# Kernel optimization log

Measured on AMD Instinct MI355X. Metric: run time of the kernel, lower is better.

Reference implementation:

```python
import jax, jax.numpy as jnp
import numpy as np

B, S = 8, 2048
D_IN, D_STATE, D_OUT = 1024, 1024, 1024
H = 16
DH = D_STATE // H  # 64
N_LAYERS = 24
STD = 0.02
EPS = 1e-6


def setup_inputs() -> dict:
    key = jax.random.key(0)
    k = jax.random.split(key, 4)
    x = jax.random.normal(k[0], (B, S, D_IN), dtype=jnp.float32)
    # input_projection: Linear(D_IN, 4*D_STATE, bias=False), std=0.02
    w_in = jax.random.normal(k[1], (D_IN, 4 * D_STATE), dtype=jnp.float32) * STD
    # state_weight: [3*H, DH, DH] recurrence matrices (candidate, forget, reset)
    state_weight = jax.random.normal(k[2], (3 * H, DH, DH), dtype=jnp.float32) * STD
    # rmsnorm weight over state_size
    norm_weight = jnp.ones((D_STATE,), dtype=jnp.float32)
    # output_projection: Linear(D_STATE, D_OUT, bias=False), std scaled by sqrt(2*num_layers)
    w_out = jax.random.normal(k[3], (D_STATE, D_OUT), dtype=jnp.float32) * (STD / np.sqrt(2 * N_LAYERS))
    return {"x": x, "w_in": w_in, "state_weight": state_weight,
            "norm_weight": norm_weight, "w_out": w_out}


def _rmsnorm(x, w):
    var = jnp.mean(jnp.square(x), axis=-1, keepdims=True)
    return x * jax.lax.rsqrt(var + EPS) * w


def reference(x, w_in, state_weight, norm_weight, w_out):
    # input projection -> [B, S, 4*D_STATE]
    proj = jnp.einsum('bsi,io->bso', x, w_in)
    xg, g = jnp.split(proj, [3 * D_STATE], axis=-1)
    xi, xf, xr = jnp.split(xg, 3, axis=-1)
    # per-head views [B, S, H, DH]
    xi = xi.reshape(B, S, H, DH)
    xf = xf.reshape(B, S, H, DH)
    xr = xr.reshape(B, S, H, DH)
    W, Wf, Wr = jnp.split(state_weight, 3, axis=0)  # each [H, DH, DH]

    # scan over time: carry h [B, H, DH]
    def step(h, inp):
        xi_t, xf_t, xr_t = inp  # each [B, H, DH]
        r = jax.nn.sigmoid(xr_t + jnp.einsum('bhd,hde->bhe', h, Wr))
        f = jax.nn.sigmoid(xf_t + jnp.einsum('bhd,hde->bhe', h, Wf))
        c = jnp.tanh(xi_t + jnp.einsum('bhd,hde->bhe', r * h, W))
        h_new = f * h + (1.0 - f) * c
        return h_new, h_new

    h0 = jnp.zeros((B, H, DH), dtype=x.dtype)
    xs = (jnp.swapaxes(xi, 0, 1), jnp.swapaxes(xf, 0, 1), jnp.swapaxes(xr, 0, 1))
    _, hs = jax.lax.scan(step, h0, xs)  # hs: [S, B, H, DH]
    h_seq = jnp.swapaxes(hs, 0, 1).reshape(B, S, D_STATE)

    # gated output: h * silu(g), rmsnorm, output projection
    y = h_seq * jax.nn.silu(g)
    y = _rmsnorm(y, norm_weight)
    return jnp.einsum('bsd,do->bso', y, w_out)
```

## Files before the change

### kernel.cpp

```cpp
#include <hip/hip_runtime.h>
#include <hip/hip_bf16.h>
#include <math.h>

typedef __hip_bfloat16 bf16;

#define B_      8
#define S_      2048
#define DIN     1024
#define DSTATE  1024
#define H_      16
#define DH_     64
#define PROJ4   4096

__device__ __forceinline__ unsigned short f2bf(float f) {
    unsigned int x = __float_as_uint(f);
    x += 0x7FFFu + ((x >> 16) & 1u);
    return (unsigned short)(x >> 16);
}

__device__ __forceinline__ float4 load4(const float* p) { return *(const float4*)p; }
__device__ __forceinline__ float4 load4(const bf16* p) {
    uint2 u = *(const uint2*)p;
    float4 r;
    r.x = __uint_as_float((u.x & 0xFFFFu) << 16);
    r.y = __uint_as_float(u.x & 0xFFFF0000u);
    r.z = __uint_as_float((u.y & 0xFFFFu) << 16);
    r.w = __uint_as_float(u.y & 0xFFFF0000u);
    return r;
}
__device__ __forceinline__ void store4(float* p, float4 v) { *(float4*)p = v; }
__device__ __forceinline__ void store4(bf16* p, float4 v) {
    uint2 u;
    u.x = (unsigned int)f2bf(v.x) | ((unsigned int)f2bf(v.y) << 16);
    u.y = (unsigned int)f2bf(v.z) | ((unsigned int)f2bf(v.w) << 16);
    *(uint2*)p = u;
}

typedef __attribute__((ext_vector_type(8))) short bf16x8;
typedef __attribute__((ext_vector_type(4))) float f32x4;
typedef __attribute__((ext_vector_type(2))) float f32x2;
typedef __attribute__((ext_vector_type(4))) short short4v;

template <typename TA>
__device__ __forceinline__ void load_a4(const TA* p, float out[4]);
template <>
__device__ __forceinline__ void load_a4<float>(const float* p, float out[4]) {
    float4 v = *(const float4*)p;
    out[0] = v.x; out[1] = v.y; out[2] = v.z; out[3] = v.w;
}
template <>
__device__ __forceinline__ void load_a4<bf16>(const bf16* p, float out[4]) {
    float4 v = load4(p);
    out[0] = v.x; out[1] = v.y; out[2] = v.z; out[3] = v.w;
}

template <typename TA, typename TC>
__global__ __launch_bounds__(256) void gemm_mfma(const TA* __restrict__ A,
                                                 const float* __restrict__ Bm,
                                                 TC* __restrict__ C,
                                                 int M, int N, int K, int lda) {
    __shared__ short As[128][40];
    __shared__ short Bs[128][40];

    const int tid = threadIdx.x;
    const int m0 = blockIdx.y * 128;
    const int n0 = blockIdx.x * 128;

    const int saM = tid >> 1;
    const int saK = (tid & 1) * 16;
    const int sbK = tid >> 3;
    const int sbN = (tid & 7) * 16;

    const int wid = tid >> 6;
    const int wx = wid & 1, wy = wid >> 1;
    const int lane = tid & 63;
    const int c16 = lane & 15;
    const int quad = lane >> 4;

    const TA* Aptr = A + (size_t)(m0 + saM) * lda + saK;
    const float* Bptr = Bm + (size_t)sbK * N + n0 + sbN;

    f32x4 acc[4][4];
    #pragma unroll
    for (int i = 0; i < 4; ++i)
        #pragma unroll
        for (int j = 0; j < 4; ++j) acc[i][j] = (f32x4){0.f, 0.f, 0.f, 0.f};

    float ra[4][4];
    float rb[4][4];
    #pragma unroll
    for (int i = 0; i < 4; ++i) load_a4<TA>(Aptr + i * 4, ra[i]);
    #pragma unroll
    for (int i = 0; i < 4; ++i) {
        float4 v = load4(Bptr + i * 4);
        rb[i][0] = v.x; rb[i][1] = v.y; rb[i][2] = v.z; rb[i][3] = v.w;
    }

    for (int k0 = 0; k0 < K; k0 += 32) {
        __syncthreads();
        #pragma unroll
        for (int i = 0; i < 4; ++i) {
            short4v pk = { (short)f2bf(ra[i][0]), (short)f2bf(ra[i][1]),
                           (short)f2bf(ra[i][2]), (short)f2bf(ra[i][3]) };
            *(short4v*)&As[saM][saK + i * 4] = pk;
        }
        #pragma unroll
        for (int i = 0; i < 4; ++i)
            #pragma unroll
            for (int j = 0; j < 4; ++j)
                Bs[sbN + i * 4 + j][sbK] = (short)f2bf(rb[i][j]);
        __syncthreads();

        if (k0 + 32 < K) {
            #pragma unroll
            for (int i = 0; i < 4; ++i) load_a4<TA>(Aptr + k0 + 32 + i * 4, ra[i]);
            #pragma unroll
            for (int i = 0; i < 4; ++i) {
                float4 v = load4(Bptr + (size_t)(k0 + 32) * N + i * 4);
                rb[i][0] = v.x; rb[i][1] = v.y; rb[i][2] = v.z; rb[i][3] = v.w;
            }
        }

        bf16x8 af[4], bfr[4];
        #pragma unroll
        for (int mt = 0; mt < 4; ++mt)
            af[mt] = *(const bf16x8*)&As[wy * 64 + mt * 16 + c16][quad * 8];
        #pragma unroll
        for (int nt = 0; nt < 4; ++nt)
            bfr[nt] = *(const bf16x8*)&Bs[wx * 64 + nt * 16 + c16][quad * 8];

        #pragma unroll
        for (int mt = 0; mt < 4; ++mt)
            #pragma unroll
            for (int nt = 0; nt < 4; ++nt)
                acc[mt][nt] = __builtin_amdgcn_mfma_f32_16x16x32_bf16(
                    af[mt], bfr[nt], acc[mt][nt], 0, 0, 0);
    }

    #pragma unroll
    for (int mt = 0; mt < 4; ++mt) {
        #pragma unroll
        for (int r = 0; r < 4; ++r) {
            int row = m0 + wy * 64 + mt * 16 + quad * 4 + r;
            TC* cp = C + (size_t)row * N + n0 + wx * 64;
            #pragma unroll
            for (int nt = 0; nt < 4; ++nt)
                cp[nt * 16 + c16] = (TC)acc[mt][nt][r];
        }
    }
}

#define RPT32(M) M(0) M(1) M(2) M(3) M(4) M(5) M(6) M(7) M(8) M(9) M(10) M(11) \
  M(12) M(13) M(14) M(15) M(16) M(17) M(18) M(19) M(20) M(21) M(22) M(23) \
  M(24) M(25) M(26) M(27) M(28) M(29) M(30) M(31)

__global__ __launch_bounds__(64, 1) void recur_kernel(bf16* __restrict__ proj,
                                                      const float* __restrict__ sw) {
    const int e = threadIdx.x & 63;
    const int bh = blockIdx.x;
    const int b = bh >> 4;
    const int h = bh & 15;

    __shared__ __align__(16) float lds_h[64];
    __shared__ __align__(16) float lds_rh[64];

    const float* Wc_p = sw + (size_t)h * 4096 + e;
    const float* Wf_p = Wc_p + (size_t)16 * 4096;
    const float* Wr_p = Wc_p + (size_t)32 * 4096;

    #define DECLW(i) f32x2 wr##i, wf##i, wc##i;
    RPT32(DECLW)
    #undef DECLW
    #define LOADW(i) \
        wr##i = (f32x2){Wr_p[(2*i) * 64], Wr_p[(2*i+1) * 64]}; \
        wf##i = (f32x2){Wf_p[(2*i) * 64], Wf_p[(2*i+1) * 64]}; \
        wc##i = (f32x2){Wc_p[(2*i) * 64], Wc_p[(2*i+1) * 64]};
    RPT32(LOADW)
    #undef LOADW

    bf16* xi_p = proj + (size_t)b * S_ * PROJ4 + h * 64 + e;

    f32x4 rxi, rxf, rxr;
    #define PRELOAD(U) { const bf16* p = xi_p + (size_t)(U) * PROJ4; \
        rxi[U] = __bfloat162float(p[0]); \
        rxf[U] = __bfloat162float(p[1024]); \
        rxr[U] = __bfloat162float(p[2048]); }
    PRELOAD(0) PRELOAD(1) PRELOAD(2) PRELOAD(3)
    #undef PRELOAD

    float hreg = 0.0f;
    lds_h[e] = 0.0f;

    const bf16* ld = xi_p + (size_t)4 * PROJ4;
    bf16*       st = xi_p;

    #define P1(J, A, Bq) { \
        f32x4 hb = *(const f32x4*)&lds_h[4 * (J)]; \
        aR0 = __builtin_elementwise_fma(hb.lo, wr##A, aR0); \
        aR1 = __builtin_elementwise_fma(hb.hi, wr##Bq, aR1); \
        aF0 = __builtin_elementwise_fma(hb.lo, wf##A, aF0); \
        aF1 = __builtin_elementwise_fma(hb.hi, wf##Bq, aF1); }
    #define P1_ALL \
        P1(0,0,1)   P1(1,2,3)   P1(2,4,5)   P1(3,6,7) \
        P1(4,8,9)   P1(5,10,11) P1(6,12,13) P1(7,14,15) \
        P1(8,16,17) P1(9,18,19) P1(10,20,21) P1(11,22,23) \
        P1(12,24,25) P1(13,26,27) P1(14,28,29) P1(15,30,31)

    #define P2(J, A, Bq) { \
        f32x4 qb = *(const f32x4*)&lds_rh[4 * (J)]; \
        aC0 = __builtin_elementwise_fma(qb.lo, wc##A, aC0); \
        aC1 = __builtin_elementwise_fma(qb.hi, wc##Bq, aC1); }
    #define P2_ALL \
        P2(0,0,1)   P2(1,2,3)   P2(2,4,5)   P2(3,6,7) \
        P2(4,8,9)   P2(5,10,11) P2(6,12,13) P2(7,14,15) \
        P2(8,16,17) P2(9,18,19) P2(10,20,21) P2(11,22,23) \
        P2(12,24,25) P2(13,26,27) P2(14,28,29) P2(15,30,31)

    #define STEP(U, REFILL) { \
        float xi0 = rxi[U], xf0 = rxf[U], xr0 = rxr[U]; \
        if (REFILL) { \
            const bf16* p = ld + (size_t)(U) * PROJ4; \
            rxi[U] = __bfloat162float(p[0]); \
            rxf[U] = __bfloat162float(p[1024]); \
            rxr[U] = __bfloat162float(p[2048]); \
        } \
        f32x2 aR0 = {0.f, 0.f}, aR1 = {0.f, 0.f}; \
        f32x2 aF0 = {0.f, 0.f}, aF1 = {0.f, 0.f}; \
        P1_ALL \
        f32x2 aR = aR0 + aR1, aF = aF0 + aF1; \
        float sr = xr0 + aR.x + aR.y; \
        float sf = xf0 + aF.x + aF.y; \
        float r = 1.f / (1.f + __expf(-sr)); \
        float f = 1.f / (1.f + __expf(-sf)); \
        float rh = r * hreg; \
        lds_rh[e] = rh; \
        f32x2 aC0 = {0.f, 0.f}, aC1 = {0.f, 0.f}; \
        P2_ALL \
        f32x2 aC = aC0 + aC1; \
        float sc = xi0 + aC.x + aC.y; \
        sc = fminf(fmaxf(sc, -15.f), 15.f); \
        float ex = __expf(-2.f * sc); \
        float cc = (1.f - ex) / (1.f + ex); \
        hreg = f * hreg + (1.f - f) * cc; \
        lds_h[e] = hreg; \
        st[(size_t)(U) * PROJ4] = __float2bfloat16(hreg); \
    }

    for (int t0 = 0; t0 < S_ - 4; t0 += 4) {
        STEP(0, 1) STEP(1, 1) STEP(2, 1) STEP(3, 1)
        ld += (size_t)4 * PROJ4;
        st += (size_t)4 * PROJ4;
    }
    STEP(0, 0) STEP(1, 0) STEP(2, 0) STEP(3, 0)

    #undef STEP
    #undef P1
    #undef P1_ALL
    #undef P2
    #undef P2_ALL
}

__global__ __launch_bounds__(256) void gate_norm_kernel(bf16* __restrict__ proj,
                                                        const float* __restrict__ nw) {
    const int row = blockIdx.x;
    const int tid = threadIdx.x;
    __shared__ float red[4];

    bf16* hp = proj + (size_t)row * PROJ4;
    const bf16* gp = hp + 3 * DSTATE;

    float4 hv = load4(hp + tid * 4);
    float4 gv = load4(gp + tid * 4);

    float v0 = hv.x * (gv.x / (1.f + __expf(-gv.x)));
    float v1 = hv.y * (gv.y / (1.f + __expf(-gv.y)));
    float v2 = hv.z * (gv.z / (1.f + __expf(-gv.z)));
    float v3 = hv.w * (gv.w / (1.f + __expf(-gv.w)));

    float ss = v0 * v0 + v1 * v1 + v2 * v2 + v3 * v3;
    #pragma unroll
    for (int mask = 32; mask >= 1; mask >>= 1)
        ss += __shfl_xor(ss, mask, 64);

    const int wid = tid >> 6;
    if ((tid & 63) == 0) red[wid] = ss;
    __syncthreads();
    float tot = red[0] + red[1] + red[2] + red[3];
    float scale = rsqrtf(tot * (1.0f / (float)DSTATE) + 1e-6f);

    float4 nv = *(const float4*)(nw + tid * 4);
    float4 y;
    y.x = v0 * scale * nv.x;
    y.y = v1 * scale * nv.y;
    y.z = v2 * scale * nv.z;
    y.w = v3 * scale * nv.w;
    store4(hp + tid * 4, y);
}

extern "C" void kernel_launch(void* const* d_in, const int* in_sizes, int n_in,
                              void* d_out, int out_size, void* d_ws, size_t ws_size,
                              hipStream_t stream) {
    const float* x     = (const float*)d_in[0];
    const float* w_in  = (const float*)d_in[1];
    const float* sw    = (const float*)d_in[2];
    const float* nw    = (const float*)d_in[3];
    const float* w_out = (const float*)d_in[4];
    float* out = (float*)d_out;

    bf16* proj = (bf16*)d_ws;

    dim3 g1(PROJ4 / 128, (B_ * S_) / 128);
    gemm_mfma<float, bf16><<<g1, 256, 0, stream>>>(x, w_in, proj,
                                                   B_ * S_, PROJ4, DIN, DIN);

    recur_kernel<<<128, 64, 0, stream>>>(proj, sw);

    gate_norm_kernel<<<B_ * S_, 256, 0, stream>>>(proj, nw);

    dim3 g2(DSTATE / 128, (B_ * S_) / 128);
    gemm_mfma<bf16, float><<<g2, 256, 0, stream>>>(proj, w_out, out,
                                                   B_ * S_, DSTATE, DSTATE, PROJ4);
}
```

Measured before the change: 1.680 ms.

## Split recurrence reduction across four waves with readlane broadcast and LDS partials

The recurrence kernel now launches 256 threads per (batch, head) instead of 64. Each wave owns 16 of the 64 input dimensions, broadcasts hidden-state values through v_readlane instead of LDS loads, and combines per-wave partial sums through LDS with two barriers per time step. The aim is to cut the serial FMA chain per step by a factor of four and add parallelism to the latency-bound scan. In exchange it adds two workgroup barriers per step plus scalar readlane overhead, and every wave recomputes the gate nonlinearities redundantly.

```diff
diff --git a/kernel.cpp b/kernel.cpp
--- a/kernel.cpp
+++ b/kernel.cpp
@@ -11,6 +11,8 @@
 #define H_      16
 #define DH_     64
 #define PROJ4   4096
+
+#define BARRIER_LGKM() asm volatile("s_waitcnt lgkmcnt(0)\n\ts_barrier" ::: "memory")
 
 __device__ __forceinline__ unsigned short f2bf(float f) {
     unsigned int x = __float_as_uint(f);
@@ -150,32 +152,37 @@
     }
 }
 
-#define RPT32(M) M(0) M(1) M(2) M(3) M(4) M(5) M(6) M(7) M(8) M(9) M(10) M(11) \
-  M(12) M(13) M(14) M(15) M(16) M(17) M(18) M(19) M(20) M(21) M(22) M(23) \
-  M(24) M(25) M(26) M(27) M(28) M(29) M(30) M(31)
-
-__global__ __launch_bounds__(64, 1) void recur_kernel(bf16* __restrict__ proj,
-                                                      const float* __restrict__ sw) {
-    const int e = threadIdx.x & 63;
+__device__ __forceinline__ float lane_bcast(float v, int lane) {
+    return __int_as_float(__builtin_amdgcn_readlane(__float_as_int(v), lane));
+}
+
+#define RPT16(M) M(0) M(1) M(2) M(3) M(4) M(5) M(6) M(7) \
+                 M(8) M(9) M(10) M(11) M(12) M(13) M(14) M(15)
+
+__global__ __launch_bounds__(256, 1) void recur_kernel(bf16* __restrict__ proj,
+                                                       const float* __restrict__ sw) {
+    const int tid = threadIdx.x;
+    const int e = tid & 63;
+    const int w = __builtin_amdgcn_readfirstlane(tid >> 6);
+    const int d0 = w << 4;
     const int bh = blockIdx.x;
     const int b = bh >> 4;
     const int h = bh & 15;
 
-    __shared__ __align__(16) float lds_h[64];
-    __shared__ __align__(16) float lds_rh[64];
-
-    const float* Wc_p = sw + (size_t)h * 4096 + e;
+    __shared__ float2 part_rf[4][64];
+    __shared__ float  part_c[4][64];
+
+    const float* Wc_p = sw + (size_t)h * 4096 + (size_t)d0 * 64 + e;
     const float* Wf_p = Wc_p + (size_t)16 * 4096;
     const float* Wr_p = Wc_p + (size_t)32 * 4096;
 
-    #define DECLW(i) f32x2 wr##i, wf##i, wc##i;
-    RPT32(DECLW)
+    #define DECLW(i) float wc##i, wf##i, wr##i;
+    RPT16(DECLW)
     #undef DECLW
-    #define LOADW(i) \
-        wr##i = (f32x2){Wr_p[(2*i) * 64], Wr_p[(2*i+1) * 64]}; \
-        wf##i = (f32x2){Wf_p[(2*i) * 64], Wf_p[(2*i+1) * 64]}; \
-        wc##i = (f32x2){Wc_p[(2*i) * 64], Wc_p[(2*i+1) * 64]};
-    RPT32(LOADW)
+    #define LOADW(i) wc##i = Wc_p[(i) * 64]; \
+                     wf##i = Wf_p[(i) * 64]; \
+                     wr##i = Wr_p[(i) * 64];
+    RPT16(LOADW)
     #undef LOADW
 
     bf16* xi_p = proj + (size_t)b * S_ * PROJ4 + h * 64 + e;
@@ -189,32 +196,15 @@
     #undef PRELOAD
 
     float hreg = 0.0f;
-    lds_h[e] = 0.0f;
 
     const bf16* ld = xi_p + (size_t)4 * PROJ4;
     bf16*       st = xi_p;
 
-    #define P1(J, A, Bq) { \
-        f32x4 hb = *(const f32x4*)&lds_h[4 * (J)]; \
-        aR0 = __builtin_elementwise_fma(hb.lo, wr##A, aR0); \
-        aR1 = __builtin_elementwise_fma(hb.hi, wr##Bq, aR1); \
-        aF0 = __builtin_elementwise_fma(hb.lo, wf##A, aF0); \
-        aF1 = __builtin_elementwise_fma(hb.hi, wf##Bq, aF1); }
-    #define P1_ALL \
-        P1(0,0,1)   P1(1,2,3)   P1(2,4,5)   P1(3,6,7) \
-        P1(4,8,9)   P1(5,10,11) P1(6,12,13) P1(7,14,15) \
-        P1(8,16,17) P1(9,18,19) P1(10,20,21) P1(11,22,23) \
-        P1(12,24,25) P1(13,26,27) P1(14,28,29) P1(15,30,31)
-
-    #define P2(J, A, Bq) { \
-        f32x4 qb = *(const f32x4*)&lds_rh[4 * (J)]; \
-        aC0 = __builtin_elementwise_fma(qb.lo, wc##A, aC0); \
-        aC1 = __builtin_elementwise_fma(qb.hi, wc##Bq, aC1); }
-    #define P2_ALL \
-        P2(0,0,1)   P2(1,2,3)   P2(2,4,5)   P2(3,6,7) \
-        P2(4,8,9)   P2(5,10,11) P2(6,12,13) P2(7,14,15) \
-        P2(8,16,17) P2(9,18,19) P2(10,20,21) P2(11,22,23) \
-        P2(12,24,25) P2(13,26,27) P2(14,28,29) P2(15,30,31)
+    #define P1T(i, A) { float hb = lane_bcast(hreg, d0 + (i)); \
+        aR##A = fmaf(hb, wr##i, aR##A); \
+        aF##A = fmaf(hb, wf##i, aF##A); }
+    #define P2T(i, A) { float qb = lane_bcast(rh, d0 + (i)); \
+        aC##A = fmaf(qb, wc##i, aC##A); }
 
     #define STEP(U, REFILL) { \
         float xi0 = rxi[U], xf0 = rxf[U], xr0 = rxr[U]; \
@@ -224,26 +214,34 @@
             rxf[U] = __bfloat162float(p[1024]); \
             rxr[U] = __bfloat162float(p[2048]); \
         } \
-        f32x2 aR0 = {0.f, 0.f}, aR1 = {0.f, 0.f}; \
-        f32x2 aF0 = {0.f, 0.f}, aF1 = {0.f, 0.f}; \
-        P1_ALL \
-        f32x2 aR = aR0 + aR1, aF = aF0 + aF1; \
-        float sr = xr0 + aR.x + aR.y; \
-        float sf = xf0 + aF.x + aF.y; \
+        float aR0 = 0.f, aR1 = 0.f, aF0 = 0.f, aF1 = 0.f; \
+        P1T(0,0)  P1T(1,1)  P1T(2,0)  P1T(3,1) \
+        P1T(4,0)  P1T(5,1)  P1T(6,0)  P1T(7,1) \
+        P1T(8,0)  P1T(9,1)  P1T(10,0) P1T(11,1) \
+        P1T(12,0) P1T(13,1) P1T(14,0) P1T(15,1) \
+        part_rf[w][e] = make_float2(aR0 + aR1, aF0 + aF1); \
+        BARRIER_LGKM(); \
+        float2 p0 = part_rf[0][e], p1 = part_rf[1][e]; \
+        float2 p2 = part_rf[2][e], p3 = part_rf[3][e]; \
+        float sr = xr0 + (p0.x + p1.x) + (p2.x + p3.x); \
+        float sf = xf0 + (p0.y + p1.y) + (p2.y + p3.y); \
         float r = 1.f / (1.f + __expf(-sr)); \
         float f = 1.f / (1.f + __expf(-sf)); \
         float rh = r * hreg; \
-        lds_rh[e] = rh; \
-        f32x2 aC0 = {0.f, 0.f}, aC1 = {0.f, 0.f}; \
-        P2_ALL \
-        f32x2 aC = aC0 + aC1; \
-        float sc = xi0 + aC.x + aC.y; \
+        float aC0 = 0.f, aC1 = 0.f; \
+        P2T(0,0)  P2T(1,1)  P2T(2,0)  P2T(3,1) \
+        P2T(4,0)  P2T(5,1)  P2T(6,0)  P2T(7,1) \
+        P2T(8,0)  P2T(9,1)  P2T(10,0) P2T(11,1) \
+        P2T(12,0) P2T(13,1) P2T(14,0) P2T(15,1) \
+        part_c[w][e] = aC0 + aC1; \
+        BARRIER_LGKM(); \
+        float sc = xi0 + (part_c[0][e] + part_c[1][e]) \
+                       + (part_c[2][e] + part_c[3][e]); \
         sc = fminf(fmaxf(sc, -15.f), 15.f); \
         float ex = __expf(-2.f * sc); \
         float cc = (1.f - ex) / (1.f + ex); \
         hreg = f * hreg + (1.f - f) * cc; \
-        lds_h[e] = hreg; \
-        st[(size_t)(U) * PROJ4] = __float2bfloat16(hreg); \
+        if (w == (U)) st[(size_t)(U) * PROJ4] = __float2bfloat16(hreg); \
     }
 
     for (int t0 = 0; t0 < S_ - 4; t0 += 4) {
@@ -254,10 +252,8 @@
     STEP(0, 0) STEP(1, 0) STEP(2, 0) STEP(3, 0)
 
     #undef STEP
-    #undef P1
-    #undef P1_ALL
-    #undef P2
-    #undef P2_ALL
+    #undef P1T
+    #undef P2T
 }
 
 __global__ __launch_bounds__(256) void gate_norm_kernel(bf16* __restrict__ proj,
@@ -313,7 +309,7 @@
     gemm_mfma<float, bf16><<<g1, 256, 0, stream>>>(x, w_in, proj,
                                                    B_ * S_, PROJ4, DIN, DIN);
 
-    recur_kernel<<<128, 64, 0, stream>>>(proj, sw);
+    recur_kernel<<<128, 256, 0, stream>>>(proj, sw);
 
     gate_norm_kernel<<<B_ * S_, 256, 0, stream>>>(proj, nw);
 
```

Result: slower. 1.744 ms (+3.8%).
